# Kernel tuning notes

Hardware: AMD Instinct MI355X
Metric: run time of the kernel (lower is better)

Reference implementation:

```python
import jax, jax.numpy as jnp
import numpy as np

DIM = 256
HEADS = 4
WIN = 128
PAD = (WIN - 1) // 2  # 63
SHIFT = WIN // 2      # 64
RED = 16              # SE reduction


def _hann(w):
    # torch.hann_window(w, periodic=False)
    n = jnp.arange(w, dtype=jnp.float32)
    return 0.5 * (1.0 - jnp.cos(2.0 * jnp.pi * n / (w - 1)))


def _layernorm(x, g, b, eps=1e-5):
    mu = jnp.mean(x, axis=-1, keepdims=True)
    var = jnp.var(x, axis=-1, keepdims=True)
    return (x - mu) * jax.lax.rsqrt(var + eps) * g + b


def _attend_windows(x, ln_g, ln_b, in_proj_w, in_proj_b, out_w, out_b):
    B, T, C = x.shape
    w = WIN
    h = HEADS
    d = C // h
    L = T + 2 * PAD - w + 1  # number of stride-1 windows (= T-1 for even w)
    y = _layernorm(x, ln_g, ln_b)
    y_pad = jnp.pad(y, ((0, 0), (PAD, PAD), (0, 0)))
    idx = jnp.arange(L)[:, None] + jnp.arange(w)[None, :]  # (L, w)
    win = y_pad[:, idx, :]  # (B, L, w, C) -- the unfold blowup
    win = win * _hann(w)[None, None, :, None]
    # fused qkv projection (torch MHA in_proj)
    qkv = jnp.einsum('blwc,ec->blwe', win, in_proj_w) + in_proj_b  # (B,L,w,3C)
    q, k, v = jnp.split(qkv, 3, axis=-1)
    q = q.reshape(B, L, w, h, d)
    k = k.reshape(B, L, w, h, d)
    v = v.reshape(B, L, w, h, d)
    scale = 1.0 / jnp.sqrt(jnp.asarray(d, dtype=x.dtype))
    scores = jnp.einsum('blqhd,blkhd->blhqk', q, k) * scale
    attn = jax.nn.softmax(scores, axis=-1)
    o = jnp.einsum('blhqk,blkhd->blqhd', attn, v).reshape(B, L, w, C)
    o = jnp.einsum('blwc,ec->blwe', o, out_w) + out_b  # out_proj
    # fold: overlap-add back to length T (crop padding)
    idx_flat = idx.reshape(-1)  # (L*w,)
    acc = jnp.zeros((B, T + 2 * PAD, C), dtype=x.dtype)
    acc = acc.at[:, idx_flat, :].add(o.reshape(B, L * w, C))
    y_out = acc[:, PAD:PAD + T, :]
    counts = jnp.zeros((T + 2 * PAD,), dtype=x.dtype).at[idx_flat].add(1.0)
    counts = counts[PAD:PAD + T]
    return y_out / (counts[None, :, None] + 1e-6)


def setup_inputs() -> dict:
    key = jax.random.key(0)
    ks = jax.random.split(key, 9)
    C = DIM
    s = 0.02
    return {
        'x': jax.random.normal(ks[0], (1, 1024, C), dtype=jnp.float32),
        'ln_g': jnp.ones((C,), jnp.float32),
        'ln_b': jnp.zeros((C,), jnp.float32),
        'in_proj_w': jax.random.normal(ks[1], (3 * C, C), jnp.float32) * s,
        'in_proj_b': jnp.zeros((3 * C,), jnp.float32),
        'out_w': jax.random.normal(ks[2], (C, C), jnp.float32) * s,
        'out_b': jnp.zeros((C,), jnp.float32),
        'proj_w': jax.random.normal(ks[3], (C, C), jnp.float32) * s,
        'proj_b': jnp.zeros((C,), jnp.float32),
        'se_w1': jax.random.normal(ks[4], (C // RED, C), jnp.float32) * s,
        'se_w2': jax.random.normal(ks[5], (C, C // RED), jnp.float32) * s,
    }


def reference(x, ln_g, ln_b, in_proj_w, in_proj_b, out_w, out_b, proj_w, proj_b, se_w1, se_w2):
    # T > window_size branch (1024 > 128)
    y_main = _attend_windows(x, ln_g, ln_b, in_proj_w, in_proj_b, out_w, out_b)
    x_shift = jnp.roll(x, SHIFT, axis=1)
    y_shift = _attend_windows(x_shift, ln_g, ln_b, in_proj_w, in_proj_b, out_w, out_b)
    y_shift = jnp.roll(y_shift, -SHIFT, axis=1)
    y = 0.5 * (y_main + y_shift)
    y = jnp.einsum('btc,ec->bte', y, proj_w) + proj_b  # proj (dropout p=0 -> identity)
    # SE module: global average over T, bottleneck MLP, sigmoid gate
    s = jnp.mean(y, axis=1)  # (B, C)
    s = jax.nn.relu(s @ se_w1.T)
    s = jax.nn.sigmoid(s @ se_w2.T)
    y = y * s[:, None, :]
    return x + y
```

## Files before the change

kernel.cpp:

```cpp
#include <hip/hip_runtime.h>

#define TLEN 1024
#define CDIM 256
#define NHEAD 4
#define HD 64
#define WIN_ 128
#define PADL 63
#define LWIN 1023
#define TPAD 1150
#define SW 32

typedef __attribute__((ext_vector_type(8))) short bf16x8;
typedef __attribute__((ext_vector_type(4))) float f32x4;

__device__ __forceinline__ int prow(int v, int t) {
  if (v == 0) return t;
  if (t < PADL || t >= PADL + TLEN) return t;
  int s = t - PADL;
  s = (s + (TLEN - 64)) & (TLEN - 1);
  return PADL + s;
}

__device__ __forceinline__ float hannf(int j) {
  return 0.5f * (1.0f - __cosf(6.283185307179586f * (float)j / 127.0f));
}

__device__ __forceinline__ float countf(int t) {
  int lo = t - 127; if (lo < 0) lo = 0;
  int hi = t;       if (hi > LWIN - 1) hi = LWIN - 1;
  return (float)(hi - lo + 1);
}

__device__ __forceinline__ unsigned short bfr(float f) {
  unsigned int u = __float_as_uint(f);
  u += 0x7FFFu + ((u >> 16) & 1u);
  return (unsigned short)(u >> 16);
}
__device__ __forceinline__ unsigned int pk2t(float a, float b) {
  return __builtin_amdgcn_perm(__float_as_uint(b), __float_as_uint(a), 0x07060302u);
}
__device__ __forceinline__ float bfu(unsigned short u) {
  return __uint_as_float(((unsigned int)u) << 16);
}
__device__ __forceinline__ float bflo(unsigned int u) { return __uint_as_float(u << 16); }
__device__ __forceinline__ float bfhi(unsigned int u) { return __uint_as_float(u & 0xFFFF0000u); }

__global__ void k_prep(const float* __restrict__ x, const float* __restrict__ g,
                       const float* __restrict__ b, unsigned short* __restrict__ lnbf,
                       const float* __restrict__ W, unsigned short* __restrict__ Wb,
                       const float* __restrict__ pw, const float* __restrict__ ow,
                       const float* __restrict__ ob, unsigned short* __restrict__ Mtb,
                       float* __restrict__ vbv,
                       float* __restrict__ accg, unsigned short* __restrict__ Pbf,
                       float* __restrict__ msum) {
  __shared__ float pr[256];
  __shared__ float red[256];
  const int bid = blockIdx.x;
  const int tid = threadIdx.x;
  if (bid < 256) {
    int wv = tid >> 6, lane = tid & 63;
    int r = bid * 4 + wv;
    float4 v = ((const float4*)(x + (size_t)r * CDIM))[lane];
    float s = v.x + v.y + v.z + v.w;
    float q = v.x * v.x + v.y * v.y + v.z * v.z + v.w * v.w;
    #pragma unroll
    for (int m = 32; m >= 1; m >>= 1) { s += __shfl_xor(s, m); q += __shfl_xor(q, m); }
    float mu = s * (1.0f / 256.0f);
    float var = q * (1.0f / 256.0f) - mu * mu;
    float rs = rsqrtf(var + 1e-5f);
    float4 gg = ((const float4*)g)[lane];
    float4 bb = ((const float4*)b)[lane];
    uint2 o;
    o.x = (unsigned int)bfr((v.x - mu) * rs * gg.x + bb.x) |
          ((unsigned int)bfr((v.y - mu) * rs * gg.y + bb.y) << 16);
    o.y = (unsigned int)bfr((v.z - mu) * rs * gg.z + bb.z) |
          ((unsigned int)bfr((v.w - mu) * rs * gg.w + bb.w) << 16);
    ((uint2*)(lnbf + (size_t)r * CDIM))[lane] = o;
  } else if (bid < 352) {
    int i = (bid - 256) * 256 + tid;
    const float4* src = (const float4*)W;
    float4 a = src[2 * i], c = src[2 * i + 1];
    uint4 o;
    o.x = (unsigned int)bfr(a.x) | ((unsigned int)bfr(a.y) << 16);
    o.y = (unsigned int)bfr(a.z) | ((unsigned int)bfr(a.w) << 16);
    o.z = (unsigned int)bfr(c.x) | ((unsigned int)bfr(c.y) << 16);
    o.w = (unsigned int)bfr(c.z) | ((unsigned int)bfr(c.w) << 16);
    ((uint4*)Wb)[i] = o;
  } else if (bid < 608) {
    const int e = bid - 352;
    pr[tid] = pw[(size_t)e * CDIM + tid];
    __syncthreads();
    float a0 = 0.f, a1 = 0.f, a2 = 0.f, a3 = 0.f;
    for (int m = 0; m < 256; m += 4) {
      a0 += pr[m] * ow[(size_t)m * CDIM + tid];
      a1 += pr[m + 1] * ow[(size_t)(m + 1) * CDIM + tid];
      a2 += pr[m + 2] * ow[(size_t)(m + 2) * CDIM + tid];
      a3 += pr[m + 3] * ow[(size_t)(m + 3) * CDIM + tid];
    }
    Mtb[(size_t)e * CDIM + tid] = bfr((a0 + a1) + (a2 + a3));
    red[tid] = pr[tid] * ob[tid];
    __syncthreads();
    for (int s = 128; s > 0; s >>= 1) { if (tid < s) red[tid] += red[tid + s]; __syncthreads(); }
    if (tid == 0) vbv[e] = red[0];
  } else if (bid < 624) {
    uint4 zz = make_uint4(0, 0, 0, 0);
    for (int i = (bid - 608) * 256 + tid; i < 147200; i += 16 * 256)
      ((uint4*)accg)[i] = zz;
  } else {
    uint4 zz = make_uint4(0, 0, 0, 0);
    for (int i = (bid - 624) * 256 + tid; i < 12096; i += 16 * 256) {
      int idx = (i < 6048) ? i : (104352 + (i - 6048));
      ((uint4*)Pbf)[idx] = zz;
    }
    if (bid == 624 && tid < 64) ((float4*)msum)[tid] = make_float4(0.f, 0.f, 0.f, 0.f);
  }
}

__launch_bounds__(512, 1)
__global__ void k_proj(const unsigned short* __restrict__ lnbf,
                       const unsigned short* __restrict__ Wb,
                       unsigned short* __restrict__ Pbf) {
  const int tid = threadIdx.x;
  const int lane = tid & 63, wv = tid >> 6;
  const int li16 = lane & 15, q4 = lane >> 4;
  const int ws = wv & 1, we = wv >> 1;
  const int s0 = blockIdx.x * 128 + ws * 64;
  const int e0 = blockIdx.y * 128 + we * 32;

  f32x4 acc[4][2];
  #pragma unroll
  for (int it = 0; it < 4; ++it)
    #pragma unroll
    for (int et = 0; et < 2; ++et) acc[it][et] = (f32x4){0.f, 0.f, 0.f, 0.f};

  #pragma unroll
  for (int ks = 0; ks < 8; ++ks) {
    bf16x8 Af[4], Bf[2];
    #pragma unroll
    for (int it = 0; it < 4; ++it)
      Af[it] = *(const bf16x8*)(lnbf + (size_t)(s0 + 16 * it + li16) * 256 + ks * 32 + q4 * 8);
    #pragma unroll
    for (int et = 0; et < 2; ++et)
      Bf[et] = *(const bf16x8*)(Wb + (size_t)(e0 + 16 * et + li16) * 256 + ks * 32 + q4 * 8);
    #pragma unroll
    for (int it = 0; it < 4; ++it)
      #pragma unroll
      for (int et = 0; et < 2; ++et)
        acc[it][et] = __builtin_amdgcn_mfma_f32_16x16x32_bf16(Af[it], Bf[et], acc[it][et], 0, 0, 0);
  }
  #pragma unroll
  for (int it = 0; it < 4; ++it)
    #pragma unroll
    for (int et = 0; et < 2; ++et)
      #pragma unroll
      for (int r = 0; r < 4; ++r) {
        int srow = s0 + 16 * it + 4 * q4 + r;
        int e = e0 + 16 * et + li16;
        Pbf[(size_t)(PADL + srow) * 768 + e] = bfr(acc[it][et][r]);
      }
}

__device__ __forceinline__ void stage_v(const unsigned short* __restrict__ Pbf,
                                        unsigned short* vt, int v, int hd,
                                        int l0, int w, int tid,
                                        const float* __restrict__ bB,
                                        const float* __restrict__ hth) {
  const int jp = tid & 63;
  const int dg = tid >> 6;
  const int j0 = 2 * jp;
  const int p0 = w + j0;
  int row0 = prow(v, l0 + w + j0);
  int row1 = prow(v, l0 + w + j0 + 1);
  uint4 a = *(const uint4*)(Pbf + (size_t)row0 * 768 + 512 + hd * 64 + dg * 8);
  uint4 b = *(const uint4*)(Pbf + (size_t)row1 * 768 + 512 + hd * 64 + dg * 8);
  float h0 = hth[j0], h1 = hth[j0 + 1];
  float e0 = __expf(h0 * bB[p0] * 0.125f);
  float e1 = __expf(h1 * bB[p0 + 1] * 0.125f);
  float f0 = e0 * h0, f1 = e1 * h1;
  unsigned int av[4] = {a.x, a.y, a.z, a.w};
  unsigned int bv[4] = {b.x, b.y, b.z, b.w};
  #pragma unroll
  for (int q = 0; q < 4; ++q) {
    int d0 = dg * 8 + 2 * q;
    unsigned int w0 = pk2t(f0 * bflo(av[q]), f1 * bflo(bv[q]));
    unsigned int w1 = pk2t(f0 * bfhi(av[q]), f1 * bfhi(bv[q]));
    *(unsigned int*)&vt[d0 * 128 + (j0 ^ ((d0 & 7) << 3))] = w0;
    *(unsigned int*)&vt[(d0 + 1) * 128 + (j0 ^ (((d0 + 1) & 7) << 3))] = w1;
  }
  if (dg == 0) {
    *(unsigned int*)&vt[64 * 128 + j0] = pk2t(e0, e1);
  }
}

__launch_bounds__(512, 2)
__global__ void k_attn(const unsigned short* __restrict__ Pbf, const float* __restrict__ ipb,
                       float* __restrict__ accg) {
  __shared__ __align__(16) unsigned short Pq[159 * 64];
  __shared__ __align__(16) unsigned short Pk[159 * 64];
  __shared__ __align__(16) unsigned short Vt[2][80 * 128];
  __shared__ __align__(16) unsigned short Ab[128 * 128];
  __shared__ __align__(16) float accs[159 * 68];
  __shared__ float hth[128];
  __shared__ float bB[160];
  __shared__ float bqS[64];

  const int strip = blockIdx.x, hd = blockIdx.y, v = blockIdx.z;
  const int l0 = strip * SW;
  const int nw = (SW < LWIN - l0) ? SW : (LWIN - l0);
  const int span = nw - 1 + WIN_;
  const int tid = threadIdx.x;
  const int lane = tid & 63, wv = tid >> 6;
  const int li16 = lane & 15, q4 = lane >> 4;
  const int iw = 16 * wv + li16;

  for (int i = tid; i < 159 * 68; i += 512) accs[i] = 0.0f;
  if (tid < 128) hth[tid] = hannf(tid);
  if (tid < 64) bqS[tid] = ipb[hd * 64 + tid];
  for (int i = tid; i < span * 8; i += 512) {
    int t = i >> 3, dg = i & 7;
    int row = prow(v, l0 + t);
    const unsigned short* src = Pbf + (size_t)row * 768 + hd * 64;
    uint4 q = *(const uint4*)(src + dg * 8);
    uint4 k = *(const uint4*)(src + 256 + dg * 8);
    int off = (dg * 8) ^ ((t & 7) << 3);
    *(uint4*)&Pq[t * 64 + off] = q;
    *(uint4*)&Pk[t * 64 + off] = k;
  }
  {
    uint4 zz = make_uint4(0, 0, 0, 0);
    for (int i = tid; i < 480; i += 512) {
      int bidx = i / 240, k = i % 240;
      *(uint4*)&Vt[bidx][65 * 128 + k * 8] = zz;
    }
  }
  __syncthreads();

  for (int p = tid; p < span; p += 512) {
    float b = 0.0f;
    int sw = (p & 7) << 3;
    for (int d = 0; d < 64; ++d) b += bqS[d] * bfu(Pk[p * 64 + (d ^ sw)]);
    bB[p] = b;
  }
  __syncthreads();
  stage_v(Pbf, &Vt[0][0], v, hd, l0, 0, tid, bB, hth);
  __syncthreads();

  float hh[32];
  {
    const float h_i = hth[iw];
    #pragma unroll
    for (int tj = 0; tj < 8; ++tj)
      #pragma unroll
      for (int r = 0; r < 4; ++r)
        hh[tj * 4 + r] = h_i * hth[16 * tj + 4 * q4 + r] * 0.125f;
  }

  #pragma unroll 1
  for (int w = 0; w < nw; ++w) {
    bf16x8 Qf[2];
    {
      int t = w + iw, sw = (t & 7) << 3;
      Qf[0] = *(bf16x8*)&Pq[t * 64 + ((8 * q4) ^ sw)];
      Qf[1] = *(bf16x8*)&Pq[t * 64 + ((32 + 8 * q4) ^ sw)];
    }
    f32x4 S[8];
    #pragma unroll
    for (int tj = 0; tj < 8; ++tj) S[tj] = (f32x4){0.f, 0.f, 0.f, 0.f};
    #pragma unroll
    for (int tj = 0; tj < 8; ++tj) {
      int t = w + 16 * tj + li16, sw = (t & 7) << 3;
      bf16x8 Kf0 = *(bf16x8*)&Pk[t * 64 + ((8 * q4) ^ sw)];
      bf16x8 Kf1 = *(bf16x8*)&Pk[t * 64 + ((32 + 8 * q4) ^ sw)];
      S[tj] = __builtin_amdgcn_mfma_f32_16x16x32_bf16(Kf0, Qf[0], S[tj], 0, 0, 0);
      S[tj] = __builtin_amdgcn_mfma_f32_16x16x32_bf16(Kf1, Qf[1], S[tj], 0, 0, 0);
    }

    #pragma unroll
    for (int tj = 0; tj < 8; ++tj)
      #pragma unroll
      for (int r = 0; r < 4; ++r)
        S[tj][r] = __expf(hh[tj * 4 + r] * S[tj][r]);

    {
      int sw = (iw & 7) << 3;
      #pragma unroll
      for (int tj = 0; tj < 8; ++tj) {
        uint2 o;
        o.x = pk2t(S[tj][0], S[tj][1]);
        o.y = pk2t(S[tj][2], S[tj][3]);
        *(uint2*)&Ab[iw * 128 + ((16 * tj + 4 * q4) ^ sw)] = o;
      }
    }

    f32x4 O[5];
    #pragma unroll
    for (int mt = 0; mt < 5; ++mt) O[mt] = (f32x4){0.f, 0.f, 0.f, 0.f};
    const unsigned short* vt = &Vt[w & 1][0];
    {
      int swi = (iw & 7) << 3;
      #pragma unroll
      for (int ks = 0; ks < 4; ++ks) {
        bf16x8 Bf = *(bf16x8*)&Ab[iw * 128 + ((32 * ks + 8 * q4) ^ swi)];
        #pragma unroll
        for (int mt = 0; mt < 5; ++mt) {
          int d = 16 * mt + li16;
          bf16x8 Af = *(bf16x8*)&vt[d * 128 + ((32 * ks + 8 * q4) ^ ((d & 7) << 3))];
          O[mt] = __builtin_amdgcn_mfma_f32_16x16x32_bf16(Af, Bf, O[mt], 0, 0, 0);
        }
      }
    }

    float nn = __shfl(O[4][0], li16);
    float sc = 1.0f / nn;

    {
      float* arow = &accs[(w + iw) * 68];
      #pragma unroll
      for (int mt = 0; mt < 4; ++mt) {
        int c = 16 * mt + 4 * q4;
        float4 cur = *(float4*)&arow[c];
        cur.x += O[mt][0] * sc; cur.y += O[mt][1] * sc;
        cur.z += O[mt][2] * sc; cur.w += O[mt][3] * sc;
        *(float4*)&arow[c] = cur;
      }
    }

    if (w + 1 < nw) stage_v(Pbf, &Vt[(w + 1) & 1][0], v, hd, l0, w + 1, tid, bB, hth);
    __syncthreads();
  }

  float* av = accg + (size_t)v * TPAD * CDIM;
  for (int i = tid; i < span * 64; i += 512) {
    int p = i >> 6, dd = i & 63;
    int lo = p - 127; if (lo < 0) lo = 0;
    int hi = p; if (hi > nw - 1) hi = nw - 1;
    float cnt = (float)(hi - lo + 1);
    float bvd = ipb[512 + hd * 64 + dd];
    atomicAdd(&av[(size_t)(l0 + p) * CDIM + hd * 64 + dd],
              accs[p * 68 + dd] + cnt * bvd);
  }
}

__launch_bounds__(512, 1)
__global__ void k_comb(const float* __restrict__ accg, const unsigned short* __restrict__ Mtb,
                       const float* __restrict__ vbv, const float* __restrict__ pb,
                       float* __restrict__ z, float* __restrict__ msum) {
  __shared__ __align__(16) unsigned short Ub[128 * 264];
  __shared__ float cfA[128], cfB[128], bscL[128];
  __shared__ float msB[256];
  const int tid = threadIdx.x;
  const int lane = tid & 63, wv = tid >> 6;
  const int li16 = lane & 15, q4 = lane >> 4;
  const int tw = wv & 1, ew = wv >> 1;
  const int t0 = blockIdx.x * 128;
  const int e0 = blockIdx.y * 128;

  if (tid < 128) {
    int s = t0 + tid;
    float c0 = countf(PADL + s);
    float c1 = countf(PADL + ((s + 64) & (TLEN - 1)));
    float fA = 0.5f / (c0 + 1e-6f), fB = 0.5f / (c1 + 1e-6f);
    cfA[tid] = fA; cfB[tid] = fB;
    bscL[tid] = c0 * fA + c1 * fB;
  }
  if (tid < 256) msB[tid] = 0.0f;
  __syncthreads();

  for (int i = tid; i < 128 * 128; i += 512) {
    int rr = i >> 7, c2 = (i & 127) * 2;
    int s = t0 + rr;
    int s1 = (s + 64) & (TLEN - 1);
    float2 a0 = *(const float2*)&accg[(size_t)(PADL + s) * CDIM + c2];
    float2 a1 = *(const float2*)&accg[(size_t)TPAD * CDIM + (size_t)(PADL + s1) * CDIM + c2];
    float fA = cfA[rr], fB = cfB[rr];
    *(unsigned int*)&Ub[rr * 264 + c2] =
        pk2t(a0.x * fA + a1.x * fB, a0.y * fA + a1.y * fB);
  }
  __syncthreads();

  f32x4 acc[4][2];
  #pragma unroll
  for (int it = 0; it < 4; ++it)
    #pragma unroll
    for (int et = 0; et < 2; ++et) acc[it][et] = (f32x4){0.f, 0.f, 0.f, 0.f};
  #pragma unroll
  for (int ks = 0; ks < 8; ++ks) {
    bf16x8 Af[4], Bf[2];
    #pragma unroll
    for (int it = 0; it < 4; ++it)
      Af[it] = *(bf16x8*)&Ub[(tw * 64 + 16 * it + li16) * 264 + ks * 32 + q4 * 8];
    #pragma unroll
    for (int et = 0; et < 2; ++et)
      Bf[et] = *(const bf16x8*)(Mtb + (size_t)(e0 + ew * 32 + 16 * et + li16) * 256 + ks * 32 + q4 * 8);
    #pragma unroll
    for (int it = 0; it < 4; ++it)
      #pragma unroll
      for (int et = 0; et < 2; ++et)
        acc[it][et] = __builtin_amdgcn_mfma_f32_16x16x32_bf16(Af[it], Bf[et], acc[it][et], 0, 0, 0);
  }

  #pragma unroll
  for (int et = 0; et < 2; ++et) {
    int e = e0 + ew * 32 + 16 * et + li16;
    float vbe = vbv[e], pbe = pb[e];
    float part = 0.0f;
    #pragma unroll
    for (int it = 0; it < 4; ++it)
      #pragma unroll
      for (int r = 0; r < 4; ++r) {
        int rloc = tw * 64 + 16 * it + 4 * q4 + r;
        float val = acc[it][et][r] + bscL[rloc] * vbe + pbe;
        z[(size_t)(t0 + rloc) * CDIM + e] = val;
        part += val;
      }
    atomicAdd(&msB[e - e0 + (e0 & 128)], part);
  }
  __syncthreads();
  if (tid < 128) atomicAdd(&msum[e0 + tid], msB[tid + (e0 & 128)]);
}

__global__ void k_finalse(const float* __restrict__ x, const float* __restrict__ z,
                          const float* __restrict__ msum, const float* __restrict__ w1,
                          const float* __restrict__ w2, float* __restrict__ out) {
  __shared__ float red2[16][4];
  __shared__ float s1[16];
  __shared__ float gateS[256];
  int tid = threadIdx.x;
  int lane = tid & 63, wv = tid >> 6;
  float sm = msum[tid] * (1.0f / 1024.0f);
  #pragma unroll
  for (int r = 0; r < 16; ++r) {
    float v = sm * w1[(size_t)r * 256 + tid];
    #pragma unroll
    for (int m = 32; m >= 1; m >>= 1) v += __shfl_xor(v, m);
    if (lane == 0) red2[r][wv] = v;
  }
  __syncthreads();
  if (tid < 16) {
    float a = red2[tid][0] + red2[tid][1] + red2[tid][2] + red2[tid][3];
    s1[tid] = fmaxf(a, 0.0f);
  }
  __syncthreads();
  float gacc = 0.0f;
  #pragma unroll
  for (int i = 0; i < 16; ++i) gacc += s1[i] * w2[(size_t)tid * 16 + i];
  gateS[tid] = 1.0f / (1.0f + __expf(-gacc));
  __syncthreads();
  int i = blockIdx.x * 256 + tid;
  float4 xv = ((const float4*)x)[i];
  float4 zv = ((const float4*)z)[i];
  float4 gv = ((const float4*)gateS)[i & 63];
  float4 o;
  o.x = xv.x + zv.x * gv.x;
  o.y = xv.y + zv.y * gv.y;
  o.z = xv.z + zv.z * gv.z;
  o.w = xv.w + zv.w * gv.w;
  ((float4*)out)[i] = o;
}

extern "C" void kernel_launch(void* const* d_in, const int* in_sizes, int n_in,
                              void* d_out, int out_size, void* d_ws, size_t ws_size,
                              hipStream_t stream) {
  const float* x   = (const float*)d_in[0];
  const float* lng = (const float*)d_in[1];
  const float* lnb = (const float*)d_in[2];
  const float* ipw = (const float*)d_in[3];
  const float* ipb = (const float*)d_in[4];
  const float* ow  = (const float*)d_in[5];
  const float* ob  = (const float*)d_in[6];
  const float* pw  = (const float*)d_in[7];
  const float* pb  = (const float*)d_in[8];
  const float* w1  = (const float*)d_in[9];
  const float* w2  = (const float*)d_in[10];
  float* out = (float*)d_out;

  float* ws = (float*)d_ws;
  unsigned short* lnbf = (unsigned short*)ws;
  unsigned short* Wb   = (unsigned short*)(ws + 131072);
  unsigned short* Pbf  = (unsigned short*)(ws + 229376);
  float* accg = ws + 229376 + 441600;
  unsigned short* Mtb = (unsigned short*)(accg + 588800);
  float* vbv  = accg + 588800 + 32768;
  float* z    = vbv + 256;
  float* msum = z + 262144;

  k_prep<<<dim3(640), dim3(256), 0, stream>>>(x, lng, lnb, lnbf, ipw, Wb,
                                              pw, ow, ob, Mtb, vbv, accg, Pbf, msum);
  k_proj<<<dim3(8, 6), dim3(512), 0, stream>>>(lnbf, Wb, Pbf);
  k_attn<<<dim3(32, NHEAD, 2), dim3(512), 0, stream>>>(Pbf, ipb, accg);
  k_comb<<<dim3(8, 2), dim3(512), 0, stream>>>(accg, Mtb, vbv, pb, z, msum);
  k_finalse<<<dim3(256), dim3(256), 0, stream>>>(x, z, msum, w1, w2, out);
}
```

Before: 207.2 us.

## Halve attention block to 256 threads, each wave computing two query tiles

The windowed attention kernel now runs with 4 waves instead of 8, and each wave handles 32 query rows (two 16-row tiles) instead of 16. This lets each loaded K fragment and V fragment feed two MFMAs, halving LDS fragment reads per MFMA. V staging is split into two passes per thread to match. The cost is doubled accumulator registers per thread and fewer waves per block, so less latency hiding and lower occupancy, with launch bounds changed to (256,1).

After: 219.9 us. 1.06x slower.

```diff
diff --git a/kernel.cpp b/kernel.cpp
--- a/kernel.cpp
+++ b/kernel.cpp
@@ -166,33 +166,38 @@
                                         const float* __restrict__ bB,
                                         const float* __restrict__ hth) {
   const int jp = tid & 63;
-  const int dg = tid >> 6;
   const int j0 = 2 * jp;
   const int p0 = w + j0;
   int row0 = prow(v, l0 + w + j0);
   int row1 = prow(v, l0 + w + j0 + 1);
-  uint4 a = *(const uint4*)(Pbf + (size_t)row0 * 768 + 512 + hd * 64 + dg * 8);
-  uint4 b = *(const uint4*)(Pbf + (size_t)row1 * 768 + 512 + hd * 64 + dg * 8);
+  const unsigned short* b0 = Pbf + (size_t)row0 * 768 + 512 + hd * 64;
+  const unsigned short* b1 = Pbf + (size_t)row1 * 768 + 512 + hd * 64;
   float h0 = hth[j0], h1 = hth[j0 + 1];
   float e0 = __expf(h0 * bB[p0] * 0.125f);
   float e1 = __expf(h1 * bB[p0 + 1] * 0.125f);
   float f0 = e0 * h0, f1 = e1 * h1;
-  unsigned int av[4] = {a.x, a.y, a.z, a.w};
-  unsigned int bv[4] = {b.x, b.y, b.z, b.w};
-  #pragma unroll
-  for (int q = 0; q < 4; ++q) {
-    int d0 = dg * 8 + 2 * q;
-    unsigned int w0 = pk2t(f0 * bflo(av[q]), f1 * bflo(bv[q]));
-    unsigned int w1 = pk2t(f0 * bfhi(av[q]), f1 * bfhi(bv[q]));
-    *(unsigned int*)&vt[d0 * 128 + (j0 ^ ((d0 & 7) << 3))] = w0;
-    *(unsigned int*)&vt[(d0 + 1) * 128 + (j0 ^ (((d0 + 1) & 7) << 3))] = w1;
-  }
-  if (dg == 0) {
+  #pragma unroll
+  for (int pass = 0; pass < 2; ++pass) {
+    int dg = (tid >> 6) + 4 * pass;
+    uint4 a = *(const uint4*)(b0 + dg * 8);
+    uint4 b = *(const uint4*)(b1 + dg * 8);
+    unsigned int av[4] = {a.x, a.y, a.z, a.w};
+    unsigned int bv[4] = {b.x, b.y, b.z, b.w};
+    #pragma unroll
+    for (int q = 0; q < 4; ++q) {
+      int d0 = dg * 8 + 2 * q;
+      unsigned int w0 = pk2t(f0 * bflo(av[q]), f1 * bflo(bv[q]));
+      unsigned int w1 = pk2t(f0 * bfhi(av[q]), f1 * bfhi(bv[q]));
+      *(unsigned int*)&vt[d0 * 128 + (j0 ^ ((d0 & 7) << 3))] = w0;
+      *(unsigned int*)&vt[(d0 + 1) * 128 + (j0 ^ (((d0 + 1) & 7) << 3))] = w1;
+    }
+  }
+  if (tid < 64) {
     *(unsigned int*)&vt[64 * 128 + j0] = pk2t(e0, e1);
   }
 }
 
-__launch_bounds__(512, 2)
+__launch_bounds__(256, 1)
 __global__ void k_attn(const unsigned short* __restrict__ Pbf, const float* __restrict__ ipb,
                        float* __restrict__ accg) {
   __shared__ __align__(16) unsigned short Pq[159 * 64];
@@ -211,12 +216,12 @@
   const int tid = threadIdx.x;
   const int lane = tid & 63, wv = tid >> 6;
   const int li16 = lane & 15, q4 = lane >> 4;
-  const int iw = 16 * wv + li16;
-
-  for (int i = tid; i < 159 * 68; i += 512) accs[i] = 0.0f;
+  const int i0 = 32 * wv + li16;
+
+  for (int i = tid; i < 159 * 68; i += 256) accs[i] = 0.0f;
   if (tid < 128) hth[tid] = hannf(tid);
   if (tid < 64) bqS[tid] = ipb[hd * 64 + tid];
-  for (int i = tid; i < span * 8; i += 512) {
+  for (int i = tid; i < span * 8; i += 256) {
     int t = i >> 3, dg = i & 7;
     int row = prow(v, l0 + t);
     const unsigned short* src = Pbf + (size_t)row * 768 + hd * 64;
@@ -228,14 +233,14 @@
   }
   {
     uint4 zz = make_uint4(0, 0, 0, 0);
-    for (int i = tid; i < 480; i += 512) {
+    for (int i = tid; i < 480; i += 256) {
       int bidx = i / 240, k = i % 240;
       *(uint4*)&Vt[bidx][65 * 128 + k * 8] = zz;
     }
   }
   __syncthreads();
 
-  for (int p = tid; p < span; p += 512) {
+  for (int p = tid; p < span; p += 256) {
     float b = 0.0f;
     int sw = (p & 7) << 3;
     for (int d = 0; d < 64; ++d) b += bqS[d] * bfu(Pk[p * 64 + (d ^ sw)]);
@@ -245,82 +250,92 @@
   stage_v(Pbf, &Vt[0][0], v, hd, l0, 0, tid, bB, hth);
   __syncthreads();
 
-  float hh[32];
-  {
-    const float h_i = hth[iw];
-    #pragma unroll
-    for (int tj = 0; tj < 8; ++tj)
-      #pragma unroll
-      for (int r = 0; r < 4; ++r)
-        hh[tj * 4 + r] = h_i * hth[16 * tj + 4 * q4 + r] * 0.125f;
-  }
+  float hhj[32];
+  #pragma unroll
+  for (int tj = 0; tj < 8; ++tj)
+    #pragma unroll
+    for (int r = 0; r < 4; ++r)
+      hhj[tj * 4 + r] = hth[16 * tj + 4 * q4 + r] * 0.125f;
+  const float hi0 = hth[i0];
+  const float hi1 = hth[i0 + 16];
 
   #pragma unroll 1
   for (int w = 0; w < nw; ++w) {
-    bf16x8 Qf[2];
-    {
-      int t = w + iw, sw = (t & 7) << 3;
-      Qf[0] = *(bf16x8*)&Pq[t * 64 + ((8 * q4) ^ sw)];
-      Qf[1] = *(bf16x8*)&Pq[t * 64 + ((32 + 8 * q4) ^ sw)];
-    }
-    f32x4 S[8];
-    #pragma unroll
-    for (int tj = 0; tj < 8; ++tj) S[tj] = (f32x4){0.f, 0.f, 0.f, 0.f};
+    bf16x8 Qf[2][2];
+    #pragma unroll
+    for (int it = 0; it < 2; ++it) {
+      int t = w + i0 + 16 * it, sw = (t & 7) << 3;
+      Qf[it][0] = *(bf16x8*)&Pq[t * 64 + ((8 * q4) ^ sw)];
+      Qf[it][1] = *(bf16x8*)&Pq[t * 64 + ((32 + 8 * q4) ^ sw)];
+    }
+    f32x4 S[2][8];
+    #pragma unroll
+    for (int it = 0; it < 2; ++it)
+      #pragma unroll
+      for (int tj = 0; tj < 8; ++tj) S[it][tj] = (f32x4){0.f, 0.f, 0.f, 0.f};
     #pragma unroll
     for (int tj = 0; tj < 8; ++tj) {
       int t = w + 16 * tj + li16, sw = (t & 7) << 3;
       bf16x8 Kf0 = *(bf16x8*)&Pk[t * 64 + ((8 * q4) ^ sw)];
       bf16x8 Kf1 = *(bf16x8*)&Pk[t * 64 + ((32 + 8 * q4) ^ sw)];
-      S[tj] = __builtin_amdgcn_mfma_f32_16x16x32_bf16(Kf0, Qf[0], S[tj], 0, 0, 0);
-      S[tj] = __builtin_amdgcn_mfma_f32_16x16x32_bf16(Kf1, Qf[1], S[tj], 0, 0, 0);
-    }
-
-    #pragma unroll
-    for (int tj = 0; tj < 8; ++tj)
-      #pragma unroll
-      for (int r = 0; r < 4; ++r)
-        S[tj][r] = __expf(hh[tj * 4 + r] * S[tj][r]);
-
-    {
-      int sw = (iw & 7) << 3;
+      S[0][tj] = __builtin_amdgcn_mfma_f32_16x16x32_bf16(Kf0, Qf[0][0], S[0][tj], 0, 0, 0);
+      S[0][tj] = __builtin_amdgcn_mfma_f32_16x16x32_bf16(Kf1, Qf[0][1], S[0][tj], 0, 0, 0);
+      S[1][tj] = __builtin_amdgcn_mfma_f32_16x16x32_bf16(Kf0, Qf[1][0], S[1][tj], 0, 0, 0);
+      S[1][tj] = __builtin_amdgcn_mfma_f32_16x16x32_bf16(Kf1, Qf[1][1], S[1][tj], 0, 0, 0);
+    }
+
+    #pragma unroll
+    for (int it = 0; it < 2; ++it) {
+      const float hi = it ? hi1 : hi0;
+      const int irow = i0 + 16 * it;
+      const int sw = (irow & 7) << 3;
       #pragma unroll
       for (int tj = 0; tj < 8; ++tj) {
+        #pragma unroll
+        for (int r = 0; r < 4; ++r)
+          S[it][tj][r] = __expf(hi * hhj[tj * 4 + r] * S[it][tj][r]);
         uint2 o;
-        o.x = pk2t(S[tj][0], S[tj][1]);
-        o.y = pk2t(S[tj][2], S[tj][3]);
-        *(uint2*)&Ab[iw * 128 + ((16 * tj + 4 * q4) ^ sw)] = o;
+        o.x = pk2t(S[it][tj][0], S[it][tj][1]);
+        o.y = pk2t(S[it][tj][2], S[it][tj][3]);
+        *(uint2*)&Ab[irow * 128 + ((16 * tj + 4 * q4) ^ sw)] = o;
       }
     }
 
-    f32x4 O[5];
-    #pragma unroll
-    for (int mt = 0; mt < 5; ++mt) O[mt] = (f32x4){0.f, 0.f, 0.f, 0.f};
+    f32x4 O[2][5];
+    #pragma unroll
+    for (int it = 0; it < 2; ++it)
+      #pragma unroll
+      for (int mt = 0; mt < 5; ++mt) O[it][mt] = (f32x4){0.f, 0.f, 0.f, 0.f};
     const unsigned short* vt = &Vt[w & 1][0];
     {
-      int swi = (iw & 7) << 3;
+      const int sw0 = (i0 & 7) << 3;
       #pragma unroll
       for (int ks = 0; ks < 4; ++ks) {
-        bf16x8 Bf = *(bf16x8*)&Ab[iw * 128 + ((32 * ks + 8 * q4) ^ swi)];
+        bf16x8 Bf0 = *(bf16x8*)&Ab[i0 * 128 + ((32 * ks + 8 * q4) ^ sw0)];
+        bf16x8 Bf1 = *(bf16x8*)&Ab[(i0 + 16) * 128 + ((32 * ks + 8 * q4) ^ sw0)];
         #pragma unroll
         for (int mt = 0; mt < 5; ++mt) {
           int d = 16 * mt + li16;
           bf16x8 Af = *(bf16x8*)&vt[d * 128 + ((32 * ks + 8 * q4) ^ ((d & 7) << 3))];
-          O[mt] = __builtin_amdgcn_mfma_f32_16x16x32_bf16(Af, Bf, O[mt], 0, 0, 0);
+          O[0][mt] = __builtin_amdgcn_mfma_f32_16x16x32_bf16(Af, Bf0, O[0][mt], 0, 0, 0);
+          O[1][mt] = __builtin_amdgcn_mfma_f32_16x16x32_bf16(Af, Bf1, O[1][mt], 0, 0, 0);
         }
       }
     }
 
-    float nn = __shfl(O[4][0], li16);
-    float sc = 1.0f / nn;
-
-    {
-      float* arow = &accs[(w + iw) * 68];
+    float sc0 = 1.0f / __shfl(O[0][4][0], li16);
+    float sc1 = 1.0f / __shfl(O[1][4][0], li16);
+
+    #pragma unroll
+    for (int it = 0; it < 2; ++it) {
+      const float sc = it ? sc1 : sc0;
+      float* arow = &accs[(w + i0 + 16 * it) * 68];
       #pragma unroll
       for (int mt = 0; mt < 4; ++mt) {
         int c = 16 * mt + 4 * q4;
         float4 cur = *(float4*)&arow[c];
-        cur.x += O[mt][0] * sc; cur.y += O[mt][1] * sc;
-        cur.z += O[mt][2] * sc; cur.w += O[mt][3] * sc;
+        cur.x += O[it][mt][0] * sc; cur.y += O[it][mt][1] * sc;
+        cur.z += O[it][mt][2] * sc; cur.w += O[it][mt][3] * sc;
         *(float4*)&arow[c] = cur;
       }
     }
@@ -330,7 +345,7 @@
   }
 
   float* av = accg + (size_t)v * TPAD * CDIM;
-  for (int i = tid; i < span * 64; i += 512) {
+  for (int i = tid; i < span * 64; i += 256) {
     int p = i >> 6, dd = i & 63;
     int lo = p - 127; if (lo < 0) lo = 0;
     int hi = p; if (hi > nw - 1) hi = nw - 1;
@@ -487,7 +502,7 @@
   k_prep<<<dim3(640), dim3(256), 0, stream>>>(x, lng, lnb, lnbf, ipw, Wb,
                                               pw, ow, ob, Mtb, vbv, accg, Pbf, msum);
   k_proj<<<dim3(8, 6), dim3(512), 0, stream>>>(lnbf, Wb, Pbf);
-  k_attn<<<dim3(32, NHEAD, 2), dim3(512), 0, stream>>>(Pbf, ipb, accg);
+  k_attn<<<dim3(32, NHEAD, 2), dim3(256), 0, stream>>>(Pbf, ipb, accg);
   k_comb<<<dim3(8, 2), dim3(512), 0, stream>>>(accg, Mtb, vbv, pb, z, msum);
   k_finalse<<<dim3(256), dim3(256), 0, stream>>>(x, z, msum, w1, w2, out);
 }
```

## Shrink proj/comb tiles for more blocks and stage proj output through LDS

Applied to the files above, without the earlier changes.

k_proj now uses 64-row tiles, giving 96 blocks instead of 48, and stages its bf16 results in shared memory so global stores are coalesced 16-byte writes. k_comb is retiled to 32 rows per block, giving 64 blocks instead of 16, with each wave computing a 16-column slice. Both changes aim to fill more of the GPU's compute units in these small GEMMs. The cost is more redundant weight loads and more msum atomics. The stage_v condition is also rewritten equivalently.

Result: faster. 192.5 us (-7.1%).

```diff
diff --git a/kernel.cpp b/kernel.cpp
--- a/kernel.cpp
+++ b/kernel.cpp
@@ -120,44 +120,52 @@
 __global__ void k_proj(const unsigned short* __restrict__ lnbf,
                        const unsigned short* __restrict__ Wb,
                        unsigned short* __restrict__ Pbf) {
+  __shared__ __align__(16) unsigned short Ps[64 * 128];
   const int tid = threadIdx.x;
   const int lane = tid & 63, wv = tid >> 6;
   const int li16 = lane & 15, q4 = lane >> 4;
   const int ws = wv & 1, we = wv >> 1;
-  const int s0 = blockIdx.x * 128 + ws * 64;
-  const int e0 = blockIdx.y * 128 + we * 32;
-
-  f32x4 acc[4][2];
-  #pragma unroll
-  for (int it = 0; it < 4; ++it)
+  const int sbase = blockIdx.x * 64;
+  const int ebase = blockIdx.y * 128;
+  const int s0 = sbase + ws * 32;
+  const int e0 = ebase + we * 32;
+
+  f32x4 acc[2][2];
+  #pragma unroll
+  for (int it = 0; it < 2; ++it)
     #pragma unroll
     for (int et = 0; et < 2; ++et) acc[it][et] = (f32x4){0.f, 0.f, 0.f, 0.f};
 
   #pragma unroll
   for (int ks = 0; ks < 8; ++ks) {
-    bf16x8 Af[4], Bf[2];
-    #pragma unroll
-    for (int it = 0; it < 4; ++it)
+    bf16x8 Af[2], Bf[2];
+    #pragma unroll
+    for (int it = 0; it < 2; ++it)
       Af[it] = *(const bf16x8*)(lnbf + (size_t)(s0 + 16 * it + li16) * 256 + ks * 32 + q4 * 8);
     #pragma unroll
     for (int et = 0; et < 2; ++et)
       Bf[et] = *(const bf16x8*)(Wb + (size_t)(e0 + 16 * et + li16) * 256 + ks * 32 + q4 * 8);
     #pragma unroll
-    for (int it = 0; it < 4; ++it)
+    for (int it = 0; it < 2; ++it)
       #pragma unroll
       for (int et = 0; et < 2; ++et)
         acc[it][et] = __builtin_amdgcn_mfma_f32_16x16x32_bf16(Af[it], Bf[et], acc[it][et], 0, 0, 0);
   }
   #pragma unroll
-  for (int it = 0; it < 4; ++it)
+  for (int it = 0; it < 2; ++it)
     #pragma unroll
     for (int et = 0; et < 2; ++et)
       #pragma unroll
       for (int r = 0; r < 4; ++r) {
-        int srow = s0 + 16 * it + 4 * q4 + r;
-        int e = e0 + 16 * et + li16;
-        Pbf[(size_t)(PADL + srow) * 768 + e] = bfr(acc[it][et][r]);
+        int lr = ws * 32 + 16 * it + 4 * q4 + r;
+        int lc = we * 32 + 16 * et + li16;
+        Ps[lr * 128 + lc] = bfr(acc[it][et][r]);
       }
+  __syncthreads();
+  for (int i = tid; i < 1024; i += 512) {
+    int r = i >> 4, c = (i & 15) * 8;
+    *(uint4*)(Pbf + (size_t)(PADL + sbase + r) * 768 + ebase + c) = *(uint4*)&Ps[r * 128 + c];
+  }
 }
 
 __device__ __forceinline__ void stage_v(const unsigned short* __restrict__ Pbf,
@@ -187,7 +195,7 @@
     *(unsigned int*)&vt[d0 * 128 + (j0 ^ ((d0 & 7) << 3))] = w0;
     *(unsigned int*)&vt[(d0 + 1) * 128 + (j0 ^ (((d0 + 1) & 7) << 3))] = w1;
   }
-  if (dg == 0) {
+  if (tid < 64) {
     *(unsigned int*)&vt[64 * 128 + j0] = pk2t(e0, e1);
   }
 }
@@ -341,21 +349,20 @@
   }
 }
 
-__launch_bounds__(512, 1)
+__launch_bounds__(512, 2)
 __global__ void k_comb(const float* __restrict__ accg, const unsigned short* __restrict__ Mtb,
                        const float* __restrict__ vbv, const float* __restrict__ pb,
                        float* __restrict__ z, float* __restrict__ msum) {
-  __shared__ __align__(16) unsigned short Ub[128 * 264];
-  __shared__ float cfA[128], cfB[128], bscL[128];
-  __shared__ float msB[256];
+  __shared__ __align__(16) unsigned short Ub[32 * 264];
+  __shared__ float cfA[32], cfB[32], bscL[32];
+  __shared__ float msB[128];
   const int tid = threadIdx.x;
   const int lane = tid & 63, wv = tid >> 6;
   const int li16 = lane & 15, q4 = lane >> 4;
-  const int tw = wv & 1, ew = wv >> 1;
-  const int t0 = blockIdx.x * 128;
+  const int t0 = blockIdx.x * 32;
   const int e0 = blockIdx.y * 128;
 
-  if (tid < 128) {
+  if (tid < 32) {
     int s = t0 + tid;
     float c0 = countf(PADL + s);
     float c1 = countf(PADL + ((s + 64) & (TLEN - 1)));
@@ -363,10 +370,10 @@
     cfA[tid] = fA; cfB[tid] = fB;
     bscL[tid] = c0 * fA + c1 * fB;
   }
-  if (tid < 256) msB[tid] = 0.0f;
-  __syncthreads();
-
-  for (int i = tid; i < 128 * 128; i += 512) {
+  if (tid < 128) msB[tid] = 0.0f;
+  __syncthreads();
+
+  for (int i = tid; i < 32 * 128; i += 512) {
     int rr = i >> 7, c2 = (i & 127) * 2;
     int s = t0 + rr;
     int s1 = (s + 64) & (TLEN - 1);
@@ -378,45 +385,36 @@
   }
   __syncthreads();
 
-  f32x4 acc[4][2];
-  #pragma unroll
-  for (int it = 0; it < 4; ++it)
-    #pragma unroll
-    for (int et = 0; et < 2; ++et) acc[it][et] = (f32x4){0.f, 0.f, 0.f, 0.f};
+  f32x4 acc[2];
+  acc[0] = (f32x4){0.f, 0.f, 0.f, 0.f};
+  acc[1] = (f32x4){0.f, 0.f, 0.f, 0.f};
   #pragma unroll
   for (int ks = 0; ks < 8; ++ks) {
-    bf16x8 Af[4], Bf[2];
-    #pragma unroll
-    for (int it = 0; it < 4; ++it)
-      Af[it] = *(bf16x8*)&Ub[(tw * 64 + 16 * it + li16) * 264 + ks * 32 + q4 * 8];
-    #pragma unroll
-    for (int et = 0; et < 2; ++et)
-      Bf[et] = *(const bf16x8*)(Mtb + (size_t)(e0 + ew * 32 + 16 * et + li16) * 256 + ks * 32 + q4 * 8);
-    #pragma unroll
-    for (int it = 0; it < 4; ++it)
-      #pragma unroll
-      for (int et = 0; et < 2; ++et)
-        acc[it][et] = __builtin_amdgcn_mfma_f32_16x16x32_bf16(Af[it], Bf[et], acc[it][et], 0, 0, 0);
-  }
-
-  #pragma unroll
-  for (int et = 0; et < 2; ++et) {
-    int e = e0 + ew * 32 + 16 * et + li16;
+    bf16x8 Bf = *(const bf16x8*)(Mtb + (size_t)(e0 + wv * 16 + li16) * 256 + ks * 32 + q4 * 8);
+    #pragma unroll
+    for (int it = 0; it < 2; ++it) {
+      bf16x8 Af = *(bf16x8*)&Ub[(16 * it + li16) * 264 + ks * 32 + q4 * 8];
+      acc[it] = __builtin_amdgcn_mfma_f32_16x16x32_bf16(Af, Bf, acc[it], 0, 0, 0);
+    }
+  }
+
+  {
+    int e = e0 + wv * 16 + li16;
     float vbe = vbv[e], pbe = pb[e];
     float part = 0.0f;
     #pragma unroll
-    for (int it = 0; it < 4; ++it)
+    for (int it = 0; it < 2; ++it)
       #pragma unroll
       for (int r = 0; r < 4; ++r) {
-        int rloc = tw * 64 + 16 * it + 4 * q4 + r;
-        float val = acc[it][et][r] + bscL[rloc] * vbe + pbe;
+        int rloc = 16 * it + 4 * q4 + r;
+        float val = acc[it][r] + bscL[rloc] * vbe + pbe;
         z[(size_t)(t0 + rloc) * CDIM + e] = val;
         part += val;
       }
-    atomicAdd(&msB[e - e0 + (e0 & 128)], part);
-  }
-  __syncthreads();
-  if (tid < 128) atomicAdd(&msum[e0 + tid], msB[tid + (e0 & 128)]);
+    atomicAdd(&msB[e - e0], part);
+  }
+  __syncthreads();
+  if (tid < 128) atomicAdd(&msum[e0 + tid], msB[tid]);
 }
 
 __global__ void k_finalse(const float* __restrict__ x, const float* __restrict__ z,
@@ -486,8 +484,8 @@
 
   k_prep<<<dim3(640), dim3(256), 0, stream>>>(x, lng, lnb, lnbf, ipw, Wb,
                                               pw, ow, ob, Mtb, vbv, accg, Pbf, msum);
-  k_proj<<<dim3(8, 6), dim3(512), 0, stream>>>(lnbf, Wb, Pbf);
+  k_proj<<<dim3(16, 6), dim3(512), 0, stream>>>(lnbf, Wb, Pbf);
   k_attn<<<dim3(32, NHEAD, 2), dim3(512), 0, stream>>>(Pbf, ipb, accg);
-  k_comb<<<dim3(8, 2), dim3(512), 0, stream>>>(accg, Mtb, vbv, pb, z, msum);
+  k_comb<<<dim3(32, 2), dim3(512), 0, stream>>>(accg, Mtb, vbv, pb, z, msum);
   k_finalse<<<dim3(256), dim3(256), 0, stream>>>(x, z, msum, w1, w2, out);
 }
```
